# Performance work log

Measured on AMD Instinct MI355X. Metric: run time of the kernel, lower is better.

## Reference

```python
import jax, jax.numpy as jnp
import numpy as np

K = 3          # kernel_size (hardcoded in forward)
D = 1          # dilation (hardcoded in forward)
ALPHA_3 = 1.0  # self.alpha_3
THRESH = 0.1   # self.vetorch_thresh


def unfold_wo_center(x):
    """x: (B, C, H, W) -> neighbors (B, C, K*K-1, H, W), center excluded.
    Matches F.unfold(kernel=K, dilation=D, padding same) reshaped to
    (B, C, K*K, H, W) with the center tap (index K*K//2) removed.
    Implemented as shifted views of the zero-padded input (no im2col blowup
    beyond the necessary K*K-1 copies)."""
    B, C, H, W = x.shape
    pad = (K + (D - 1) * (K - 1)) // 2
    xp = jnp.pad(x, ((0, 0), (0, 0), (pad, pad), (pad, pad)))
    offs = [(i * D, j * D) for i in range(K) for j in range(K)]
    del offs[(K * K) // 2]  # drop center -> 8 neighbors for K=3
    nbrs = jnp.stack([xp[:, :, oy:oy + H, ox:ox + W] for oy, ox in offs], axis=2)
    return nbrs  # (B, C, 8, H, W)


def _neighbor_norm(x):
    # ||x_p - x_q||_2 over channel dim -> (B, 8, H, W)
    diff = x[:, :, None] - unfold_wo_center(x)
    return jnp.sqrt(jnp.sum(diff * diff, axis=1))


def setup_inputs() -> dict:
    key = jax.random.key(0)
    k1, k2 = jax.random.split(key)
    return {
        "images_lab": jax.random.normal(k1, (16, 3, 256, 256), dtype=jnp.float32),
        "pixel_vector": jax.random.normal(k2, (16, 6, 256, 256), dtype=jnp.float32),
    }


def reference(images_lab, pixel_vector):
    # get_lab_neighbor_diff: exp(-alpha * ||lab diff||)
    W_ij = jnp.exp(-ALPHA_3 * _neighbor_norm(images_lab))   # (B, 8, H, W)
    # get_vector_neighbor_diff: ||embedding diff||
    vector_ij = _neighbor_norm(pixel_vector)                # (B, 8, H, W)
    # neighbor_loss = mean((W_ij >= thresh) * vector_ij)
    neighbor_loss = jnp.mean(
        (W_ij >= THRESH).astype(vector_ij.dtype) * vector_ij
    )
    sim_maps = jnp.concatenate([W_ij, vector_ij], axis=1)   # (B, 16, H, W)
    return sim_maps, neighbor_loss
```

## Files before the change

### kernel.cpp

```cpp
#include <hip/hip_runtime.h>

#define HWSZ 65536
#define OUT_MAPS (16 * 16 * HWSZ)
#define NBLK 512

typedef float fvec4 __attribute__((ext_vector_type(4)));

__device__ __forceinline__ void expand_row(fvec4 m, int lane, float v[6]) {
    float lft = __shfl_up(m.w, 1, 64);
    float rgt = __shfl_down(m.x, 1, 64);
    if (lane == 0)  lft = 0.f;
    if (lane == 63) rgt = 0.f;
    v[0] = lft; v[1] = m.x; v[2] = m.y; v[3] = m.z; v[4] = m.w; v[5] = rgt;
}

__global__ __launch_bounds__(256, 2) void sim_main(
    const float* __restrict__ lab,
    const float* __restrict__ vec,
    float* __restrict__ out,
    float* __restrict__ partials)
{
    const int g    = blockIdx.x * 256 + threadIdx.x;
    const int lane = threadIdx.x & 63;
    const int wv   = g >> 6;
    const int b    = wv >> 7;
    const int h0   = (wv & 127) << 1;
    const int w0   = lane << 2;

    const bool hasU = (h0 > 0);
    const bool hasD = (h0 < 254);

    constexpr int DY[8] = {-1,-1,-1, 0, 0, 1, 1, 1};
    constexpr int DX[8] = {-1, 0, 1,-1, 1,-1, 0, 1};

    const fvec4 zz = {0.f, 0.f, 0.f, 0.f};

    fvec4 L[3][4];
    fvec4 V[6][4];
    {
        const float* pl = lab + b * 3 * HWSZ + h0 * 256 + w0;
        #pragma unroll
        for (int c = 0; c < 3; ++c) {
            L[c][0] = hasU ? *reinterpret_cast<const fvec4*>(pl + c * HWSZ - 256) : zz;
            L[c][1] =        *reinterpret_cast<const fvec4*>(pl + c * HWSZ);
            L[c][2] =        *reinterpret_cast<const fvec4*>(pl + c * HWSZ + 256);
            L[c][3] = hasD ? *reinterpret_cast<const fvec4*>(pl + c * HWSZ + 512) : zz;
        }
        const float* pv = vec + b * 6 * HWSZ + h0 * 256 + w0;
        #pragma unroll
        for (int c = 0; c < 6; ++c) {
            V[c][0] = hasU ? *reinterpret_cast<const fvec4*>(pv + c * HWSZ - 256) : zz;
            V[c][1] =        *reinterpret_cast<const fvec4*>(pv + c * HWSZ);
            V[c][2] =        *reinterpret_cast<const fvec4*>(pv + c * HWSZ + 256);
            V[c][3] = hasD ? *reinterpret_cast<const fvec4*>(pv + c * HWSZ + 512) : zz;
        }
    }

    float accA[8][4], accB[8][4];
    float* ob = out + b * 16 * HWSZ + h0 * 256 + w0;

    #pragma unroll
    for (int k = 0; k < 8; ++k)
        #pragma unroll
        for (int j = 0; j < 4; ++j) { accA[k][j] = 0.f; accB[k][j] = 0.f; }

    #pragma unroll
    for (int c = 0; c < 3; ++c) {
        float v[4][6];
        #pragma unroll
        for (int r = 0; r < 4; ++r) expand_row(L[c][r], lane, v[r]);
        #pragma unroll
        for (int k = 0; k < 8; ++k) {
            const int r = DY[k] + 1, dx = DX[k];
            #pragma unroll
            for (int j = 0; j < 4; ++j) {
                const float dA = v[1][j + 1] - v[r][j + 1 + dx];
                accA[k][j] = fmaf(dA, dA, accA[k][j]);
                const float dB = v[2][j + 1] - v[r + 1][j + 1 + dx];
                accB[k][j] = fmaf(dB, dB, accB[k][j]);
            }
        }
    }

    unsigned maskA = 0, maskB = 0;
    #pragma unroll
    for (int k = 0; k < 8; ++k) {
        float wA[4], wB[4];
        #pragma unroll
        for (int j = 0; j < 4; ++j) {
            wA[j] = __expf(-__builtin_amdgcn_sqrtf(accA[k][j]));
            wB[j] = __expf(-__builtin_amdgcn_sqrtf(accB[k][j]));
            if (wA[j] >= 0.1f) maskA |= 1u << (k * 4 + j);
            if (wB[j] >= 0.1f) maskB |= 1u << (k * 4 + j);
        }
        fvec4 sA = {wA[0], wA[1], wA[2], wA[3]};
        fvec4 sB = {wB[0], wB[1], wB[2], wB[3]};
        __builtin_nontemporal_store(sA, reinterpret_cast<fvec4*>(ob + k * HWSZ));
        __builtin_nontemporal_store(sB, reinterpret_cast<fvec4*>(ob + k * HWSZ + 256));
    }

    #pragma unroll
    for (int k = 0; k < 8; ++k)
        #pragma unroll
        for (int j = 0; j < 4; ++j) { accA[k][j] = 0.f; accB[k][j] = 0.f; }

    #pragma unroll
    for (int c = 0; c < 6; ++c) {
        float v[4][6];
        #pragma unroll
        for (int r = 0; r < 4; ++r) expand_row(V[c][r], lane, v[r]);
        #pragma unroll
        for (int k = 0; k < 8; ++k) {
            const int r = DY[k] + 1, dx = DX[k];
            #pragma unroll
            for (int j = 0; j < 4; ++j) {
                const float dA = v[1][j + 1] - v[r][j + 1 + dx];
                accA[k][j] = fmaf(dA, dA, accA[k][j]);
                const float dB = v[2][j + 1] - v[r + 1][j + 1 + dx];
                accB[k][j] = fmaf(dB, dB, accB[k][j]);
            }
        }
    }

    float lsum = 0.f;
    #pragma unroll
    for (int k = 0; k < 8; ++k) {
        float vA[4], vB[4];
        #pragma unroll
        for (int j = 0; j < 4; ++j) {
            vA[j] = __builtin_amdgcn_sqrtf(accA[k][j]);
            vB[j] = __builtin_amdgcn_sqrtf(accB[k][j]);
            if (maskA & (1u << (k * 4 + j))) lsum += vA[j];
            if (maskB & (1u << (k * 4 + j))) lsum += vB[j];
        }
        fvec4 sA = {vA[0], vA[1], vA[2], vA[3]};
        fvec4 sB = {vB[0], vB[1], vB[2], vB[3]};
        __builtin_nontemporal_store(sA, reinterpret_cast<fvec4*>(ob + (8 + k) * HWSZ));
        __builtin_nontemporal_store(sB, reinterpret_cast<fvec4*>(ob + (8 + k) * HWSZ + 256));
    }

    #pragma unroll
    for (int off = 32; off > 0; off >>= 1)
        lsum += __shfl_down(lsum, off, 64);
    __shared__ float ws[4];
    const int wid = threadIdx.x >> 6;
    if (lane == 0) ws[wid] = lsum;
    __syncthreads();
    if (threadIdx.x == 0)
        partials[blockIdx.x] = ws[0] + ws[1] + ws[2] + ws[3];
}

__global__ __launch_bounds__(256) void loss_reduce(
    const float* __restrict__ partials, float* __restrict__ out_loss)
{
    float s = 0.f;
    #pragma unroll
    for (int i = 0; i < NBLK / 256; ++i)
        s += partials[i * 256 + threadIdx.x];
    #pragma unroll
    for (int off = 32; off > 0; off >>= 1)
        s += __shfl_down(s, off, 64);
    __shared__ float ws[4];
    const int lane = threadIdx.x & 63;
    const int wid  = threadIdx.x >> 6;
    if (lane == 0) ws[wid] = s;
    __syncthreads();
    if (threadIdx.x == 0)
        out_loss[0] = (ws[0] + ws[1] + ws[2] + ws[3]) / 8388608.0f;
}

extern "C" void kernel_launch(void* const* d_in, const int* in_sizes, int n_in,
                              void* d_out, int out_size, void* d_ws, size_t ws_size,
                              hipStream_t stream) {
    const float* lab = (const float*)d_in[0];
    const float* vec = (const float*)d_in[1];
    float* out      = (float*)d_out;
    float* partials = (float*)d_ws;

    sim_main<<<NBLK, 256, 0, stream>>>(lab, vec, out, partials);
    loss_reduce<<<1, 256, 0, stream>>>(partials, out + OUT_MAPS);
}
```

Before: 25.36 us.

## Fuse loss reduction into main kernel via fixed-point atomics and last-block finish

Removes the separate loss_reduce launch by having each block atomically add its partial sum, converted to 64-bit fixed point, into a workspace counter. The last block to finish, found with an atomic ticket, writes the final mean. Block indices are also swizzled so that consecutive blocks land on different XCDs. This trades a second kernel launch for a memset plus atomics, and the fixed-point scaling assumes non-negative partial sums within range.

```diff
diff --git a/kernel.cpp b/kernel.cpp
--- a/kernel.cpp
+++ b/kernel.cpp
@@ -3,6 +3,7 @@
 #define HWSZ 65536
 #define OUT_MAPS (16 * 16 * HWSZ)
 #define NBLK 512
+#define FXSCALE 16777216.0f
 
 typedef float fvec4 __attribute__((ext_vector_type(4)));
 
@@ -18,9 +19,10 @@
     const float* __restrict__ lab,
     const float* __restrict__ vec,
     float* __restrict__ out,
-    float* __restrict__ partials)
+    unsigned long long* __restrict__ acc)
 {
-    const int g    = blockIdx.x * 256 + threadIdx.x;
+    const int bs   = ((blockIdx.x & 7) << 6) | (blockIdx.x >> 3);
+    const int g    = bs * 256 + threadIdx.x;
     const int lane = threadIdx.x & 63;
     const int wv   = g >> 6;
     const int b    = wv >> 7;
@@ -146,27 +148,21 @@
     const int wid = threadIdx.x >> 6;
     if (lane == 0) ws[wid] = lsum;
     __syncthreads();
-    if (threadIdx.x == 0)
-        partials[blockIdx.x] = ws[0] + ws[1] + ws[2] + ws[3];
-}
-
-__global__ __launch_bounds__(256) void loss_reduce(
-    const float* __restrict__ partials, float* __restrict__ out_loss)
-{
-    float s = 0.f;
-    #pragma unroll
-    for (int i = 0; i < NBLK / 256; ++i)
-        s += partials[i * 256 + threadIdx.x];
-    #pragma unroll
-    for (int off = 32; off > 0; off >>= 1)
-        s += __shfl_down(s, off, 64);
-    __shared__ float ws[4];
-    const int lane = threadIdx.x & 63;
-    const int wid  = threadIdx.x >> 6;
-    if (lane == 0) ws[wid] = s;
-    __syncthreads();
-    if (threadIdx.x == 0)
-        out_loss[0] = (ws[0] + ws[1] + ws[2] + ws[3]) / 8388608.0f;
+    if (threadIdx.x == 0) {
+        const float Sb = ws[0] + ws[1] + ws[2] + ws[3];
+        const unsigned long long fx =
+            (unsigned long long)(Sb * FXSCALE + 0.5f);
+        atomicAdd(acc, fx);
+        __threadfence();
+        const unsigned int done =
+            atomicAdd(reinterpret_cast<unsigned int*>(acc + 1), 1u);
+        if (done == NBLK - 1) {
+            __threadfence();
+            const unsigned long long total = atomicAdd(acc, 0ull);
+            out[OUT_MAPS] =
+                (float)((double)total * (1.0 / (double)FXSCALE) / 8388608.0);
+        }
+    }
 }
 
 extern "C" void kernel_launch(void* const* d_in, const int* in_sizes, int n_in,
@@ -174,9 +170,9 @@
                               hipStream_t stream) {
     const float* lab = (const float*)d_in[0];
     const float* vec = (const float*)d_in[1];
-    float* out      = (float*)d_out;
-    float* partials = (float*)d_ws;
+    float* out = (float*)d_out;
+    unsigned long long* acc = (unsigned long long*)d_ws;
 
-    sim_main<<<NBLK, 256, 0, stream>>>(lab, vec, out, partials);
-    loss_reduce<<<1, 256, 0, stream>>>(partials, out + OUT_MAPS);
+    hipMemsetAsync(d_ws, 0, 16, stream);
+    sim_main<<<NBLK, 256, 0, stream>>>(lab, vec, out, acc);
 }
```

New measurement: 42.76 us. +68.6%, slower.
